# Optimization experiments

Hardware: AMD Instinct MI355X
Metric: run time of the kernel (lower is better)

## Reference

```python
import jax, jax.numpy as jnp
import numpy as np

N_ATOMS = 100000
N_BONDS = 250000
MAX_NB = 6
HIDDEN = 256
DEPTH = 3
NUM_MOLS = 2000
ATOM_FDIM = 133
BOND_FDIM = 147


def setup_inputs() -> dict:
    key = jax.random.key(0)
    ks = jax.random.split(key, 12)
    return {
        "f_atoms": jax.random.normal(ks[0], (N_ATOMS, ATOM_FDIM), jnp.float32),
        "f_bonds": jax.random.normal(ks[1], (N_BONDS, BOND_FDIM), jnp.float32),
        "w_atoms": jax.random.uniform(ks[2], (N_ATOMS,), jnp.float32),
        "w_bonds": jax.random.uniform(ks[3], (N_BONDS,), jnp.float32),
        "W_i": jax.random.normal(ks[4], (BOND_FDIM, HIDDEN), jnp.float32) * 0.05,
        "W_h": jax.random.normal(ks[5], (HIDDEN, HIDDEN), jnp.float32) * 0.05,
        "W_o": jax.random.normal(ks[6], (ATOM_FDIM + HIDDEN, HIDDEN), jnp.float32) * 0.05,
        "b_o": jnp.zeros((HIDDEN,), jnp.float32),
        "degree_of_polym": jax.random.uniform(ks[7], (NUM_MOLS,), jnp.float32),
        "a2b": jax.random.randint(ks[8], (N_ATOMS, MAX_NB), 0, N_BONDS, jnp.int32),
        "b2a": jax.random.randint(ks[9], (N_BONDS,), 0, N_ATOMS, jnp.int32),
        "b2revb": jax.random.randint(ks[10], (N_BONDS,), 0, N_BONDS, jnp.int32),
        "mol_ids": jnp.sort(jax.random.randint(ks[11], (N_ATOMS,), 0, NUM_MOLS, jnp.int32)),
    }


def reference(f_atoms, f_bonds, w_atoms, w_bonds, W_i, W_h, W_o, b_o,
              degree_of_polym, a2b, b2a, b2revb, mol_ids):
    # input-layer: bond features -> hidden messages
    inp = f_bonds @ W_i                      # [n_bonds, H]
    message = jax.nn.relu(inp)

    for _ in range(DEPTH - 1):
        # gather incoming bond messages per atom and weight them
        nei_msg = message[a2b]               # [n_atoms, max_nb, H]
        nei_w = w_bonds[a2b]                 # [n_atoms, max_nb]
        a_message = (nei_msg * nei_w[..., None]).sum(axis=1)  # [n_atoms, H]
        # directed message: total at source atom minus reverse bond
        message = a_message[b2a] - message[b2revb]             # [n_bonds, H]
        message = jax.nn.relu(inp + message @ W_h)             # dropout p=0 (eval)

    # final atom-level readout
    nei_msg = message[a2b] * w_bonds[a2b][..., None]
    a_message = nei_msg.sum(axis=1)                            # [n_atoms, H]
    a_input = jnp.concatenate([f_atoms, a_message], axis=1)    # [n_atoms, atom_fdim+H]
    atom_hiddens = jax.nn.relu(a_input @ W_o + b_o)            # [n_atoms, H]

    # per-molecule weighted mean aggregation (a_scope loop -> segment_sum)
    weighted = atom_hiddens * w_atoms[:, None]
    mol_sum = jax.ops.segment_sum(weighted, mol_ids, num_segments=NUM_MOLS)
    w_sum = jax.ops.segment_sum(w_atoms, mol_ids, num_segments=NUM_MOLS)
    safe_w = jnp.where(w_sum > 0, w_sum, 1.0)
    mol_vecs = jnp.where((w_sum > 0)[:, None], mol_sum / safe_w[:, None], 0.0)
    mol_vecs = degree_of_polym[:, None] * mol_vecs             # [num_mols, H]
    return mol_vecs
```

## Files before the change

kernel.cpp:

```cpp
#include <hip/hip_runtime.h>
#include <hip/hip_bf16.h>

typedef unsigned short u16;
typedef __bf16 bf16x8v __attribute__((ext_vector_type(8)));
typedef float f32x4v __attribute__((ext_vector_type(4)));

__device__ __forceinline__ float bf2f(u16 u) {
    union { float f; unsigned int i; } c; c.i = ((unsigned int)u) << 16; return c.f;
}
__device__ __forceinline__ u16 f2bf(float f) {
    union { float f; unsigned int i; } c; c.f = f;
    unsigned int i = c.i;
    unsigned int lsb = (i >> 16) & 1u;
    i += 0x7fffu + lsb;
    return (u16)(i >> 16);
}
__device__ __forceinline__ float lo16(unsigned u) { return bf2f((u16)(u & 0xffff)); }
__device__ __forceinline__ float hi16(unsigned u) { return bf2f((u16)(u >> 16)); }
__device__ __forceinline__ unsigned pack2(float lo, float hi) {
    return (unsigned)f2bf(lo) | ((unsigned)f2bf(hi) << 16);
}

__global__ void pack_w(const float* __restrict__ W, u16* __restrict__ Wt, int K, int Kpad) {
    int idx = blockIdx.x * 256 + threadIdx.x;
    if (idx >= 256 * Kpad) return;
    int n = idx / Kpad, k = idx % Kpad;
    float v = (k < K) ? W[k * 256 + n] : 0.f;
    Wt[idx] = f2bf(v);
}

__global__ void pack_wo(const float* __restrict__ W_o, u16* __restrict__ Wt) {
    int idx = blockIdx.x * 256 + threadIdx.x;
    if (idx >= 256 * 448) return;
    int n = idx / 448, k = idx % 448;
    float v;
    if (k < 256)       v = W_o[(133 + k) * 256 + n];
    else if (k < 389)  v = W_o[(k - 256) * 256 + n];
    else               v = 0.f;
    Wt[idx] = f2bf(v);
}

__global__ void convert_fbonds(const float* __restrict__ fb, u16* __restrict__ out, int nB) {
    int idx = blockIdx.x * 256 + threadIdx.x;
    if (idx >= nB * 192) return;
    int b = idx / 192, k = idx % 192;
    float v = (k < 147) ? fb[b * 147 + k] : 0.f;
    out[idx] = f2bf(v);
}

__global__ void convert_fatoms(const float* __restrict__ fa, u16* __restrict__ out, int nA) {
    int idx = blockIdx.x * 256 + threadIdx.x;
    if (idx >= nA * 192) return;
    int a = idx / 192, c = idx % 192;
    float v = (c < 133) ? fa[a * 133 + c] : 0.f;
    out[idx] = f2bf(v);
}

template <bool RELU>
__global__ __launch_bounds__(256)
void gather16(const u16* __restrict__ msg, const int* __restrict__ a2b,
              const float* __restrict__ w_bonds, u16* __restrict__ out, int nAtoms) {
    int t = threadIdx.x;
    int atom = blockIdx.x * 8 + (t >> 5);
    int co = (t & 31) * 8;
    if (atom >= nAtoms) return;
    float a[8] = {0.f, 0.f, 0.f, 0.f, 0.f, 0.f, 0.f, 0.f};
#pragma unroll
    for (int j = 0; j < 6; ++j) {
        int b = a2b[atom * 6 + j];
        float w = w_bonds[b];
        uint4 v = *(const uint4*)(msg + (size_t)b * 256 + co);
        unsigned p[4] = {v.x, v.y, v.z, v.w};
#pragma unroll
        for (int q = 0; q < 4; ++q) {
            float m0 = lo16(p[q]), m1 = hi16(p[q]);
            if (RELU) { m0 = fmaxf(m0, 0.f); m1 = fmaxf(m1, 0.f); }
            a[q * 2]     += w * m0;
            a[q * 2 + 1] += w * m1;
        }
    }
    uint4 o;
    o.x = pack2(a[0], a[1]); o.y = pack2(a[2], a[3]);
    o.z = pack2(a[4], a[5]); o.w = pack2(a[6], a[7]);
    *(uint4*)(out + (size_t)atom * 256 + co) = o;
}

template <bool RELU>
__global__ __launch_bounds__(256)
void direct16(const u16* __restrict__ amsg, const u16* __restrict__ msg,
              const int* __restrict__ b2a, const int* __restrict__ b2revb,
              u16* __restrict__ mdir, int nBonds) {
    int t = threadIdx.x;
    int bond = blockIdx.x * 8 + (t >> 5);
    int co = (t & 31) * 8;
    if (bond >= nBonds) return;
    int sa = b2a[bond], rb = b2revb[bond];
    uint4 va = *(const uint4*)(amsg + (size_t)sa * 256 + co);
    uint4 vr = *(const uint4*)(msg + (size_t)rb * 256 + co);
    unsigned pa[4] = {va.x, va.y, va.z, va.w};
    unsigned pr[4] = {vr.x, vr.y, vr.z, vr.w};
    uint4 o;
    unsigned po[4];
#pragma unroll
    for (int q = 0; q < 4; ++q) {
        float rl = lo16(pr[q]), rh = hi16(pr[q]);
        if (RELU) { rl = fmaxf(rl, 0.f); rh = fmaxf(rh, 0.f); }
        po[q] = pack2(lo16(pa[q]) - rl, hi16(pa[q]) - rh);
    }
    o.x = po[0]; o.y = po[1]; o.z = po[2]; o.w = po[3];
    *(uint4*)(mdir + (size_t)bond * 256 + co) = o;
}

template <int MODE, int KPAD>
__global__ __launch_bounds__(512, 2)
void gemm_full(const u16* __restrict__ A, const u16* __restrict__ Bt, int M,
               const u16* __restrict__ inp, u16* __restrict__ out0) {
    constexpr int LSTR = KPAD + 8;
    __shared__ u16 Bs[256 * LSTR];
    const int tid = threadIdx.x;
    const int wave = tid >> 6;
    const int lane = tid & 63;
    const int mrow = lane & 15;
    const int quad = lane >> 4;

    constexpr int KC = KPAD / 8;
    for (int i = tid; i < 256 * KC; i += 512) {
        int r = i / KC, kc = i % KC;
        *(uint4*)&Bs[r * LSTR + kc * 8] =
            *(const uint4*)&Bt[(size_t)r * KPAD + kc * 8];
    }
    __syncthreads();

    for (long chunk = blockIdx.x; chunk * 256 < (long)M; chunk += gridDim.x) {
        const long mbase = chunk * 256 + wave * 32;
        long row[2];
#pragma unroll
        for (int t = 0; t < 2; ++t) {
            long r = mbase + t * 16 + mrow;
            if (r >= M) r = M - 1;
            row[t] = r;
        }

        f32x4v acc[2][16];
#pragma unroll
        for (int t = 0; t < 2; ++t)
#pragma unroll
            for (int j = 0; j < 16; ++j) acc[t][j] = (f32x4v){0.f, 0.f, 0.f, 0.f};

#pragma unroll 2
        for (int k0 = 0; k0 < KPAD; k0 += 32) {
            bf16x8v a_frag[2];
#pragma unroll
            for (int t = 0; t < 2; ++t)
                a_frag[t] = *(const bf16x8v*)&A[row[t] * KPAD + k0 + quad * 8];
#pragma unroll
            for (int jg = 0; jg < 4; ++jg) {
                bf16x8v b_frag[4];
#pragma unroll
                for (int j4 = 0; j4 < 4; ++j4)
                    b_frag[j4] = *(const bf16x8v*)&Bs[((jg * 4 + j4) * 16 + mrow) * LSTR + k0 + quad * 8];
#pragma unroll
                for (int t = 0; t < 2; ++t)
#pragma unroll
                    for (int j4 = 0; j4 < 4; ++j4)
                        acc[t][jg * 4 + j4] = __builtin_amdgcn_mfma_f32_16x16x32_bf16(
                            a_frag[t], b_frag[j4], acc[t][jg * 4 + j4], 0, 0, 0);
            }
        }

#pragma unroll
        for (int t = 0; t < 2; ++t) {
#pragma unroll
            for (int r = 0; r < 4; ++r) {
                long grow = mbase + t * 16 + quad * 4 + r;
                if (grow < M) {
#pragma unroll
                    for (int j = 0; j < 16; ++j) {
                        int gcol = j * 16 + mrow;
                        size_t idx = (size_t)grow * 256 + gcol;
                        float v = acc[t][j][r];
                        if constexpr (MODE == 0) {
                            out0[idx] = f2bf(v);
                        } else {
                            float s = bf2f(inp[idx]) + v;
                            out0[idx] = f2bf(s > 0.f ? s : 0.f);
                        }
                    }
                }
            }
        }
    }
}

template <int KPAD, int KSPLIT, int NT>
__global__ __launch_bounds__(256, 3)
void gemm_stream(const u16* __restrict__ A1, const u16* __restrict__ A2,
                 const u16* __restrict__ Bt, int M,
                 const float* __restrict__ bias, float* __restrict__ outf) {
    constexpr int LSTR = KPAD + 8;
    constexpr int NROWS = NT * 16;
    constexpr int K2 = KPAD - KSPLIT;
    __shared__ u16 Bs[NROWS * LSTR];
    const int tid = threadIdx.x;
    const int wave = tid >> 6;
    const int lane = tid & 63;
    const int mrow = lane & 15;
    const int quad = lane >> 4;
    const int nbase = blockIdx.y * NROWS;

    constexpr int KC = KPAD / 8;
    for (int i = tid; i < NROWS * KC; i += 256) {
        int r = i / KC, kc = i % KC;
        *(uint4*)&Bs[r * LSTR + kc * 8] =
            *(const uint4*)&Bt[(size_t)(nbase + r) * KPAD + kc * 8];
    }
    __syncthreads();

    for (long chunk = blockIdx.x; chunk * 256 < (long)M; chunk += gridDim.x) {
        const long mbase = chunk * 256 + wave * 64;
        long row[4];
#pragma unroll
        for (int t = 0; t < 4; ++t) {
            long r = mbase + t * 16 + mrow;
            if (r >= M) r = M - 1;
            row[t] = r;
        }

        f32x4v acc[4][NT];
#pragma unroll
        for (int t = 0; t < 4; ++t)
#pragma unroll
            for (int j = 0; j < NT; ++j) acc[t][j] = (f32x4v){0.f, 0.f, 0.f, 0.f};

#pragma unroll 2
        for (int k0 = 0; k0 < KSPLIT; k0 += 32) {
            bf16x8v a_frag[4], b_frag[NT];
#pragma unroll
            for (int t = 0; t < 4; ++t)
                a_frag[t] = *(const bf16x8v*)&A1[row[t] * KSPLIT + k0 + quad * 8];
#pragma unroll
            for (int j = 0; j < NT; ++j)
                b_frag[j] = *(const bf16x8v*)&Bs[(j * 16 + mrow) * LSTR + k0 + quad * 8];
#pragma unroll
            for (int t = 0; t < 4; ++t)
#pragma unroll
                for (int j = 0; j < NT; ++j)
                    acc[t][j] = __builtin_amdgcn_mfma_f32_16x16x32_bf16(
                        a_frag[t], b_frag[j], acc[t][j], 0, 0, 0);
        }
        if constexpr (K2 > 0) {
#pragma unroll 2
            for (int k0 = 0; k0 < K2; k0 += 32) {
                bf16x8v a_frag[4], b_frag[NT];
#pragma unroll
                for (int t = 0; t < 4; ++t)
                    a_frag[t] = *(const bf16x8v*)&A2[row[t] * K2 + k0 + quad * 8];
#pragma unroll
                for (int j = 0; j < NT; ++j)
                    b_frag[j] = *(const bf16x8v*)&Bs[(j * 16 + mrow) * LSTR + KSPLIT + k0 + quad * 8];
#pragma unroll
                for (int t = 0; t < 4; ++t)
#pragma unroll
                    for (int j = 0; j < NT; ++j)
                        acc[t][j] = __builtin_amdgcn_mfma_f32_16x16x32_bf16(
                            a_frag[t], b_frag[j], acc[t][j], 0, 0, 0);
            }
        }

#pragma unroll
        for (int t = 0; t < 4; ++t) {
#pragma unroll
            for (int r = 0; r < 4; ++r) {
                long grow = mbase + t * 16 + quad * 4 + r;
                if (grow < M) {
#pragma unroll
                    for (int j = 0; j < NT; ++j) {
                        int gcol = nbase + j * 16 + mrow;
                        float s = acc[t][j][r] + bias[gcol];
                        outf[(size_t)grow * 256 + gcol] = s > 0.f ? s : 0.f;
                    }
                }
            }
        }
    }
}

__global__ __launch_bounds__(256)
void aggregate_kernel(const float* __restrict__ hid, const float* __restrict__ w_atoms,
                      const int* __restrict__ mol_ids, const float* __restrict__ deg,
                      float* __restrict__ out, int nAtoms) {
    int m = blockIdx.x;
    int t = threadIdx.x;
    int lo = 0, hi = nAtoms;
    while (lo < hi) { int mid = (lo + hi) >> 1; if (mol_ids[mid] < m) lo = mid + 1; else hi = mid; }
    int start = lo;
    lo = start; hi = nAtoms;
    while (lo < hi) { int mid = (lo + hi) >> 1; if (mol_ids[mid] < m + 1) lo = mid + 1; else hi = mid; }
    int end = lo;
    float acc = 0.f, wsum = 0.f;
    for (int a = start; a < end; ++a) {
        float w = w_atoms[a];
        wsum += w;
        acc += w * hid[(size_t)a * 256 + t];
    }
    float res = (wsum > 0.f) ? deg[m] * acc / wsum : 0.f;
    out[m * 256 + t] = res;
}

extern "C" void kernel_launch(void* const* d_in, const int* in_sizes, int n_in,
                              void* d_out, int out_size, void* d_ws, size_t ws_size,
                              hipStream_t stream) {
    const float* f_atoms = (const float*)d_in[0];
    const float* f_bonds = (const float*)d_in[1];
    const float* w_atoms = (const float*)d_in[2];
    const float* w_bonds = (const float*)d_in[3];
    const float* W_i     = (const float*)d_in[4];
    const float* W_h     = (const float*)d_in[5];
    const float* W_o     = (const float*)d_in[6];
    const float* b_o     = (const float*)d_in[7];
    const float* deg     = (const float*)d_in[8];
    const int*   a2b     = (const int*)d_in[9];
    const int*   b2a     = (const int*)d_in[10];
    const int*   b2revb  = (const int*)d_in[11];
    const int*   mol_ids = (const int*)d_in[12];
    float* out = (float*)d_out;

    const int nB = 250000, nA = 100000, nM = 2000;

    char* ws = (char*)d_ws;
    u16* inp    = (u16*)(ws);
    u16* msgA   = (u16*)(ws + 128000000L);
    u16* buf2   = (u16*)(ws + 256000000L);
    u16* amsg   = (u16*)(ws + 384000000L);
    u16* wt_i   = (u16*)(ws + 435200000L);
    u16* wt_h   = (u16*)(ws + 435200000L + 98304L);
    u16* wt_o   = (u16*)(ws + 435200000L + 98304L + 131072L);
    u16* fatoms = msgA;
    float* hid  = (float*)buf2;

    if (ws_size < 435658752UL) return;

    dim3 b256(256), b512(512);
    pack_w<<<dim3((256 * 192 + 255) / 256), b256, 0, stream>>>(W_i, wt_i, 147, 192);
    pack_w<<<dim3((256 * 256 + 255) / 256), b256, 0, stream>>>(W_h, wt_h, 256, 256);
    pack_wo<<<dim3((256 * 448 + 255) / 256), b256, 0, stream>>>(W_o, wt_o);
    convert_fbonds<<<dim3(nB * 192 / 256), b256, 0, stream>>>(f_bonds, buf2, nB);

    gemm_full<0, 192><<<dim3(256), b512, 0, stream>>>(buf2, wt_i, nB, nullptr, inp);

    gather16<true><<<dim3(nA / 8), b256, 0, stream>>>(inp, a2b, w_bonds, amsg, nA);
    direct16<true><<<dim3(nB / 8), b256, 0, stream>>>(amsg, inp, b2a, b2revb, buf2, nB);
    gemm_full<1, 256><<<dim3(256), b512, 0, stream>>>(buf2, wt_h, nB, inp, msgA);

    gather16<false><<<dim3(nA / 8), b256, 0, stream>>>(msgA, a2b, w_bonds, amsg, nA);
    direct16<false><<<dim3(nB / 8), b256, 0, stream>>>(amsg, msgA, b2a, b2revb, buf2, nB);
    gemm_full<1, 256><<<dim3(256), b512, 0, stream>>>(buf2, wt_h, nB, inp, inp);

    convert_fatoms<<<dim3(nA * 192 / 256), b256, 0, stream>>>(f_atoms, fatoms, nA);
    gather16<false><<<dim3(nA / 8), b256, 0, stream>>>(inp , a2b, w_bonds, amsg, nA);
    gemm_stream<448, 256, 4><<<dim3(128, 4), b256, 0, stream>>>(
        amsg, fatoms, wt_o, nA, b_o, hid);

    aggregate_kernel<<<dim3(nM), b256, 0, stream>>>(hid, w_atoms, mol_ids, deg, out, nA);
}
```

Baseline: 1.006 ms.

## Fuse directed-message and fp32-to-bf16 conversion into GEMM A-operand loads

Removes the standalone direct16 and convert_fbonds/convert_fatoms kernels. The GEMMs now build their A fragments on the fly: from gathered atom messages minus reverse-bond messages for the W_h steps, and from raw fp32 features converted in registers for the W_i and W_o steps. This avoids writing and re-reading several large bf16 intermediates of size bonds×256. The costs are irregular gather loads inside the MFMA loop, plus changed grid sizes and tiling (W_i K padding cut to 160, readout GEMM reshaped to 512 threads with 2×8 tiles). Both changes could affect latency hiding and occupancy.

```diff
diff --git a/kernel.cpp b/kernel.cpp
--- a/kernel.cpp
+++ b/kernel.cpp
@@ -4,6 +4,7 @@
 typedef unsigned short u16;
 typedef __bf16 bf16x8v __attribute__((ext_vector_type(8)));
 typedef float f32x4v __attribute__((ext_vector_type(4)));
+typedef float f32x4u __attribute__((ext_vector_type(4))) __attribute__((aligned(4)));
 
 __device__ __forceinline__ float bf2f(u16 u) {
     union { float f; unsigned int i; } c; c.i = ((unsigned int)u) << 16; return c.f;
@@ -19,6 +20,27 @@
 __device__ __forceinline__ float hi16(unsigned u) { return bf2f((u16)(u >> 16)); }
 __device__ __forceinline__ unsigned pack2(float lo, float hi) {
     return (unsigned)f2bf(lo) | ((unsigned)f2bf(hi) << 16);
+}
+
+__device__ __forceinline__ bf16x8v load_cvt8(const float* __restrict__ rowp, int k, int kmax) {
+    union { unsigned u[4]; bf16x8v v; } r;
+#pragma unroll
+    for (int g = 0; g < 2; ++g) {
+        int kk = k + g * 4;
+        float f0, f1, f2, f3;
+        if (kk + 3 < kmax) {
+            f32x4u q = *(const f32x4u*)(rowp + kk);
+            f0 = q.x; f1 = q.y; f2 = q.z; f3 = q.w;
+        } else {
+            f0 = (kk + 0 < kmax) ? rowp[kk + 0] : 0.f;
+            f1 = (kk + 1 < kmax) ? rowp[kk + 1] : 0.f;
+            f2 = (kk + 2 < kmax) ? rowp[kk + 2] : 0.f;
+            f3 = (kk + 3 < kmax) ? rowp[kk + 3] : 0.f;
+        }
+        r.u[g * 2]     = pack2(f0, f1);
+        r.u[g * 2 + 1] = pack2(f2, f3);
+    }
+    return r.v;
 }
 
 __global__ void pack_w(const float* __restrict__ W, u16* __restrict__ Wt, int K, int Kpad) {
@@ -40,22 +62,6 @@
     Wt[idx] = f2bf(v);
 }
 
-__global__ void convert_fbonds(const float* __restrict__ fb, u16* __restrict__ out, int nB) {
-    int idx = blockIdx.x * 256 + threadIdx.x;
-    if (idx >= nB * 192) return;
-    int b = idx / 192, k = idx % 192;
-    float v = (k < 147) ? fb[b * 147 + k] : 0.f;
-    out[idx] = f2bf(v);
-}
-
-__global__ void convert_fatoms(const float* __restrict__ fa, u16* __restrict__ out, int nA) {
-    int idx = blockIdx.x * 256 + threadIdx.x;
-    if (idx >= nA * 192) return;
-    int a = idx / 192, c = idx % 192;
-    float v = (c < 133) ? fa[a * 133 + c] : 0.f;
-    out[idx] = f2bf(v);
-}
-
 template <bool RELU>
 __global__ __launch_bounds__(256)
 void gather16(const u16* __restrict__ msg, const int* __restrict__ a2b,
@@ -85,36 +91,10 @@
     *(uint4*)(out + (size_t)atom * 256 + co) = o;
 }
 
-template <bool RELU>
-__global__ __launch_bounds__(256)
-void direct16(const u16* __restrict__ amsg, const u16* __restrict__ msg,
-              const int* __restrict__ b2a, const int* __restrict__ b2revb,
-              u16* __restrict__ mdir, int nBonds) {
-    int t = threadIdx.x;
-    int bond = blockIdx.x * 8 + (t >> 5);
-    int co = (t & 31) * 8;
-    if (bond >= nBonds) return;
-    int sa = b2a[bond], rb = b2revb[bond];
-    uint4 va = *(const uint4*)(amsg + (size_t)sa * 256 + co);
-    uint4 vr = *(const uint4*)(msg + (size_t)rb * 256 + co);
-    unsigned pa[4] = {va.x, va.y, va.z, va.w};
-    unsigned pr[4] = {vr.x, vr.y, vr.z, vr.w};
-    uint4 o;
-    unsigned po[4];
-#pragma unroll
-    for (int q = 0; q < 4; ++q) {
-        float rl = lo16(pr[q]), rh = hi16(pr[q]);
-        if (RELU) { rl = fmaxf(rl, 0.f); rh = fmaxf(rh, 0.f); }
-        po[q] = pack2(lo16(pa[q]) - rl, hi16(pa[q]) - rh);
-    }
-    o.x = po[0]; o.y = po[1]; o.z = po[2]; o.w = po[3];
-    *(uint4*)(mdir + (size_t)bond * 256 + co) = o;
-}
-
-template <int MODE, int KPAD>
 __global__ __launch_bounds__(512, 2)
-void gemm_full(const u16* __restrict__ A, const u16* __restrict__ Bt, int M,
-               const u16* __restrict__ inp, u16* __restrict__ out0) {
+void gemm_in(const float* __restrict__ A, const u16* __restrict__ Bt, int M,
+             u16* __restrict__ out0) {
+    constexpr int KPAD = 160, KMAX = 147, ASTR = 147;
     constexpr int LSTR = KPAD + 8;
     __shared__ u16 Bs[256 * LSTR];
     const int tid = threadIdx.x;
@@ -126,19 +106,18 @@
     constexpr int KC = KPAD / 8;
     for (int i = tid; i < 256 * KC; i += 512) {
         int r = i / KC, kc = i % KC;
-        *(uint4*)&Bs[r * LSTR + kc * 8] =
-            *(const uint4*)&Bt[(size_t)r * KPAD + kc * 8];
+        *(uint4*)&Bs[r * LSTR + kc * 8] = *(const uint4*)&Bt[(size_t)r * KPAD + kc * 8];
     }
     __syncthreads();
 
     for (long chunk = blockIdx.x; chunk * 256 < (long)M; chunk += gridDim.x) {
         const long mbase = chunk * 256 + wave * 32;
-        long row[2];
+        const float* rowp[2];
 #pragma unroll
         for (int t = 0; t < 2; ++t) {
             long r = mbase + t * 16 + mrow;
             if (r >= M) r = M - 1;
-            row[t] = r;
+            rowp[t] = A + r * ASTR;
         }
 
         f32x4v acc[2][16];
@@ -152,7 +131,7 @@
             bf16x8v a_frag[2];
 #pragma unroll
             for (int t = 0; t < 2; ++t)
-                a_frag[t] = *(const bf16x8v*)&A[row[t] * KPAD + k0 + quad * 8];
+                a_frag[t] = load_cvt8(rowp[t], k0 + quad * 8, KMAX);
 #pragma unroll
             for (int jg = 0; jg < 4; ++jg) {
                 bf16x8v b_frag[4];
@@ -169,37 +148,113 @@
         }
 
 #pragma unroll
-        for (int t = 0; t < 2; ++t) {
+        for (int t = 0; t < 2; ++t)
 #pragma unroll
             for (int r = 0; r < 4; ++r) {
                 long grow = mbase + t * 16 + quad * 4 + r;
-                if (grow < M) {
+                if (grow < M)
+#pragma unroll
+                    for (int j = 0; j < 16; ++j)
+                        out0[(size_t)grow * 256 + j * 16 + mrow] = f2bf(acc[t][j][r]);
+            }
+    }
+}
+
+template <bool RELUV>
+__global__ __launch_bounds__(512, 2)
+void gemm_mp(const u16* __restrict__ amsg, const u16* __restrict__ msgsrc,
+             const int* __restrict__ b2a, const int* __restrict__ b2revb,
+             const u16* __restrict__ Bt, int M,
+             const u16* __restrict__ inp, u16* __restrict__ out0) {
+    constexpr int KPAD = 256;
+    constexpr int LSTR = KPAD + 8;
+    __shared__ u16 Bs[256 * LSTR];
+    const int tid = threadIdx.x;
+    const int wave = tid >> 6;
+    const int lane = tid & 63;
+    const int mrow = lane & 15;
+    const int quad = lane >> 4;
+
+    constexpr int KC = KPAD / 8;
+    for (int i = tid; i < 256 * KC; i += 512) {
+        int r = i / KC, kc = i % KC;
+        *(uint4*)&Bs[r * LSTR + kc * 8] = *(const uint4*)&Bt[(size_t)r * KPAD + kc * 8];
+    }
+    __syncthreads();
+
+    for (long chunk = blockIdx.x; chunk * 256 < (long)M; chunk += gridDim.x) {
+        const long mbase = chunk * 256 + wave * 32;
+        size_t soff[2], roff[2];
+#pragma unroll
+        for (int t = 0; t < 2; ++t) {
+            long b = mbase + t * 16 + mrow;
+            if (b >= M) b = M - 1;
+            soff[t] = (size_t)b2a[b] * 256 + quad * 8;
+            roff[t] = (size_t)b2revb[b] * 256 + quad * 8;
+        }
+
+        f32x4v acc[2][16];
+#pragma unroll
+        for (int t = 0; t < 2; ++t)
+#pragma unroll
+            for (int j = 0; j < 16; ++j) acc[t][j] = (f32x4v){0.f, 0.f, 0.f, 0.f};
+
+#pragma unroll 2
+        for (int k0 = 0; k0 < KPAD; k0 += 32) {
+            bf16x8v a_frag[2];
+#pragma unroll
+            for (int t = 0; t < 2; ++t) {
+                uint4 va = *(const uint4*)&amsg[soff[t] + k0];
+                uint4 vr = *(const uint4*)&msgsrc[roff[t] + k0];
+                unsigned pa[4] = {va.x, va.y, va.z, va.w};
+                unsigned pr[4] = {vr.x, vr.y, vr.z, vr.w};
+                union { unsigned u[4]; bf16x8v v; } res;
+#pragma unroll
+                for (int p = 0; p < 4; ++p) {
+                    float rl = lo16(pr[p]), rh = hi16(pr[p]);
+                    if (RELUV) { rl = fmaxf(rl, 0.f); rh = fmaxf(rh, 0.f); }
+                    res.u[p] = pack2(lo16(pa[p]) - rl, hi16(pa[p]) - rh);
+                }
+                a_frag[t] = res.v;
+            }
+#pragma unroll
+            for (int jg = 0; jg < 4; ++jg) {
+                bf16x8v b_frag[4];
+#pragma unroll
+                for (int j4 = 0; j4 < 4; ++j4)
+                    b_frag[j4] = *(const bf16x8v*)&Bs[((jg * 4 + j4) * 16 + mrow) * LSTR + k0 + quad * 8];
+#pragma unroll
+                for (int t = 0; t < 2; ++t)
+#pragma unroll
+                    for (int j4 = 0; j4 < 4; ++j4)
+                        acc[t][jg * 4 + j4] = __builtin_amdgcn_mfma_f32_16x16x32_bf16(
+                            a_frag[t], b_frag[j4], acc[t][jg * 4 + j4], 0, 0, 0);
+            }
+        }
+
+#pragma unroll
+        for (int t = 0; t < 2; ++t)
+#pragma unroll
+            for (int r = 0; r < 4; ++r) {
+                long grow = mbase + t * 16 + quad * 4 + r;
+                if (grow < M)
 #pragma unroll
                     for (int j = 0; j < 16; ++j) {
-                        int gcol = j * 16 + mrow;
-                        size_t idx = (size_t)grow * 256 + gcol;
-                        float v = acc[t][j][r];
-                        if constexpr (MODE == 0) {
-                            out0[idx] = f2bf(v);
-                        } else {
-                            float s = bf2f(inp[idx]) + v;
-                            out0[idx] = f2bf(s > 0.f ? s : 0.f);
-                        }
+                        size_t idx = (size_t)grow * 256 + j * 16 + mrow;
+                        float s = bf2f(inp[idx]) + acc[t][j][r];
+                        out0[idx] = f2bf(s > 0.f ? s : 0.f);
                     }
-                }
-            }
-        }
-    }
-}
-
-template <int KPAD, int KSPLIT, int NT>
-__global__ __launch_bounds__(256, 3)
-void gemm_stream(const u16* __restrict__ A1, const u16* __restrict__ A2,
-                 const u16* __restrict__ Bt, int M,
-                 const float* __restrict__ bias, float* __restrict__ outf) {
+            }
+    }
+}
+
+__global__ __launch_bounds__(512, 2)
+void gemm_ro(const u16* __restrict__ A1, const float* __restrict__ A2,
+             const u16* __restrict__ Bt, int M,
+             const float* __restrict__ bias, float* __restrict__ outf) {
+    constexpr int KPAD = 448, KSPLIT = 256, K2 = 192, KMAX2 = 133;
     constexpr int LSTR = KPAD + 8;
-    constexpr int NROWS = NT * 16;
-    constexpr int K2 = KPAD - KSPLIT;
+    constexpr int NROWS = 128;
     __shared__ u16 Bs[NROWS * LSTR];
     const int tid = threadIdx.x;
     const int wave = tid >> 6;
@@ -209,7 +264,7 @@
     const int nbase = blockIdx.y * NROWS;
 
     constexpr int KC = KPAD / 8;
-    for (int i = tid; i < NROWS * KC; i += 256) {
+    for (int i = tid; i < NROWS * KC; i += 512) {
         int r = i / KC, kc = i % KC;
         *(uint4*)&Bs[r * LSTR + kc * 8] =
             *(const uint4*)&Bt[(size_t)(nbase + r) * KPAD + kc * 8];
@@ -217,71 +272,67 @@
     __syncthreads();
 
     for (long chunk = blockIdx.x; chunk * 256 < (long)M; chunk += gridDim.x) {
-        const long mbase = chunk * 256 + wave * 64;
-        long row[4];
-#pragma unroll
-        for (int t = 0; t < 4; ++t) {
+        const long mbase = chunk * 256 + wave * 32;
+        long row[2];
+#pragma unroll
+        for (int t = 0; t < 2; ++t) {
             long r = mbase + t * 16 + mrow;
             if (r >= M) r = M - 1;
             row[t] = r;
         }
 
-        f32x4v acc[4][NT];
-#pragma unroll
-        for (int t = 0; t < 4; ++t)
-#pragma unroll
-            for (int j = 0; j < NT; ++j) acc[t][j] = (f32x4v){0.f, 0.f, 0.f, 0.f};
+        f32x4v acc[2][8];
+#pragma unroll
+        for (int t = 0; t < 2; ++t)
+#pragma unroll
+            for (int j = 0; j < 8; ++j) acc[t][j] = (f32x4v){0.f, 0.f, 0.f, 0.f};
 
 #pragma unroll 2
         for (int k0 = 0; k0 < KSPLIT; k0 += 32) {
-            bf16x8v a_frag[4], b_frag[NT];
-#pragma unroll
-            for (int t = 0; t < 4; ++t)
+            bf16x8v a_frag[2], b_frag[8];
+#pragma unroll
+            for (int t = 0; t < 2; ++t)
                 a_frag[t] = *(const bf16x8v*)&A1[row[t] * KSPLIT + k0 + quad * 8];
 #pragma unroll
-            for (int j = 0; j < NT; ++j)
+            for (int j = 0; j < 8; ++j)
                 b_frag[j] = *(const bf16x8v*)&Bs[(j * 16 + mrow) * LSTR + k0 + quad * 8];
 #pragma unroll
-            for (int t = 0; t < 4; ++t)
-#pragma unroll
-                for (int j = 0; j < NT; ++j)
+            for (int t = 0; t < 2; ++t)
+#pragma unroll
+                for (int j = 0; j < 8; ++j)
                     acc[t][j] = __builtin_amdgcn_mfma_f32_16x16x32_bf16(
                         a_frag[t], b_frag[j], acc[t][j], 0, 0, 0);
         }
-        if constexpr (K2 > 0) {
 #pragma unroll 2
-            for (int k0 = 0; k0 < K2; k0 += 32) {
-                bf16x8v a_frag[4], b_frag[NT];
-#pragma unroll
-                for (int t = 0; t < 4; ++t)
-                    a_frag[t] = *(const bf16x8v*)&A2[row[t] * K2 + k0 + quad * 8];
-#pragma unroll
-                for (int j = 0; j < NT; ++j)
-                    b_frag[j] = *(const bf16x8v*)&Bs[(j * 16 + mrow) * LSTR + KSPLIT + k0 + quad * 8];
-#pragma unroll
-                for (int t = 0; t < 4; ++t)
-#pragma unroll
-                    for (int j = 0; j < NT; ++j)
-                        acc[t][j] = __builtin_amdgcn_mfma_f32_16x16x32_bf16(
-                            a_frag[t], b_frag[j], acc[t][j], 0, 0, 0);
-            }
-        }
-
-#pragma unroll
-        for (int t = 0; t < 4; ++t) {
+        for (int k0 = 0; k0 < K2; k0 += 32) {
+            bf16x8v a_frag[2], b_frag[8];
+#pragma unroll
+            for (int t = 0; t < 2; ++t)
+                a_frag[t] = load_cvt8(A2 + row[t] * KMAX2, k0 + quad * 8, KMAX2);
+#pragma unroll
+            for (int j = 0; j < 8; ++j)
+                b_frag[j] = *(const bf16x8v*)&Bs[(j * 16 + mrow) * LSTR + KSPLIT + k0 + quad * 8];
+#pragma unroll
+            for (int t = 0; t < 2; ++t)
+#pragma unroll
+                for (int j = 0; j < 8; ++j)
+                    acc[t][j] = __builtin_amdgcn_mfma_f32_16x16x32_bf16(
+                        a_frag[t], b_frag[j], acc[t][j], 0, 0, 0);
+        }
+
+#pragma unroll
+        for (int t = 0; t < 2; ++t)
 #pragma unroll
             for (int r = 0; r < 4; ++r) {
                 long grow = mbase + t * 16 + quad * 4 + r;
-                if (grow < M) {
-#pragma unroll
-                    for (int j = 0; j < NT; ++j) {
+                if (grow < M)
+#pragma unroll
+                    for (int j = 0; j < 8; ++j) {
                         int gcol = nbase + j * 16 + mrow;
                         float s = acc[t][j][r] + bias[gcol];
                         outf[(size_t)grow * 256 + gcol] = s > 0.f ? s : 0.f;
                     }
-                }
-            }
-        }
+            }
     }
 }
 
@@ -330,36 +381,31 @@
     char* ws = (char*)d_ws;
     u16* inp    = (u16*)(ws);
     u16* msgA   = (u16*)(ws + 128000000L);
-    u16* buf2   = (u16*)(ws + 256000000L);
+    float* hid  = (float*)(ws + 256000000L);
     u16* amsg   = (u16*)(ws + 384000000L);
     u16* wt_i   = (u16*)(ws + 435200000L);
-    u16* wt_h   = (u16*)(ws + 435200000L + 98304L);
-    u16* wt_o   = (u16*)(ws + 435200000L + 98304L + 131072L);
-    u16* fatoms = msgA;
-    float* hid  = (float*)buf2;
-
-    if (ws_size < 435658752UL) return;
+    u16* wt_h   = (u16*)(ws + 435200000L + 81920L);
+    u16* wt_o   = (u16*)(ws + 435200000L + 81920L + 131072L);
+
+    if (ws_size < 435642368UL) return;
 
     dim3 b256(256), b512(512);
-    pack_w<<<dim3((256 * 192 + 255) / 256), b256, 0, stream>>>(W_i, wt_i, 147, 192);
+    pack_w<<<dim3((256 * 160 + 255) / 256), b256, 0, stream>>>(W_i, wt_i, 147, 160);
     pack_w<<<dim3((256 * 256 + 255) / 256), b256, 0, stream>>>(W_h, wt_h, 256, 256);
     pack_wo<<<dim3((256 * 448 + 255) / 256), b256, 0, stream>>>(W_o, wt_o);
-    convert_fbonds<<<dim3(nB * 192 / 256), b256, 0, stream>>>(f_bonds, buf2, nB);
-
-    gemm_full<0, 192><<<dim3(256), b512, 0, stream>>>(buf2, wt_i, nB, nullptr, inp);
+
+    gemm_in<<<dim3(977), b512, 0, stream>>>(f_bonds, wt_i, nB, inp);
 
     gather16<true><<<dim3(nA / 8), b256, 0, stream>>>(inp, a2b, w_bonds, amsg, nA);
-    direct16<true><<<dim3(nB / 8), b256, 0, stream>>>(amsg, inp, b2a, b2revb, buf2, nB);
-    gemm_full<1, 256><<<dim3(256), b512, 0, stream>>>(buf2, wt_h, nB, inp, msgA);
+    gemm_mp<true><<<dim3(977), b512, 0, stream>>>(
+        amsg, inp, b2a, b2revb, wt_h, nB, inp, msgA);
 
     gather16<false><<<dim3(nA / 8), b256, 0, stream>>>(msgA, a2b, w_bonds, amsg, nA);
-    direct16<false><<<dim3(nB / 8), b256, 0, stream>>>(amsg, msgA, b2a, b2revb, buf2, nB);
-    gemm_full<1, 256><<<dim3(256), b512, 0, stream>>>(buf2, wt_h, nB, inp, inp);
-
-    convert_fatoms<<<dim3(nA * 192 / 256), b256, 0, stream>>>(f_atoms, fatoms, nA);
+    gemm_mp<false><<<dim3(977), b512, 0, stream>>>(
+        amsg, msgA, b2a, b2revb, wt_h, nB, inp, inp);
+
     gather16<false><<<dim3(nA / 8), b256, 0, stream>>>(inp , a2b, w_bonds, amsg, nA);
-    gemm_stream<448, 256, 4><<<dim3(128, 4), b256, 0, stream>>>(
-        amsg, fatoms, wt_o, nA, b_o, hid);
+    gemm_ro<<<dim3(391, 2), b512, 0, stream>>>(amsg, f_atoms, wt_o, nA, b_o, hid);
 
     aggregate_kernel<<<dim3(nM), b256, 0, stream>>>(hid, w_atoms, mol_ids, deg, out, nA);
 }
```

Result: faster. 852.3 us (-15.3%).
